# Kernel tuning notes

Measured on AMD Instinct MI355X. Metric: run time of the kernel, lower is better.

The kernel has to match this reference:

```python
import jax, jax.numpy as jnp
import numpy as np

SEQ_LEN = 96
D_MODEL = 512
BATCH = 512
FREQ = SEQ_LEN // 2 + 1  # 49
EPS = 1e-5


def setup_inputs() -> dict:
    key = jax.random.key(0)
    ks = jax.random.split(key, 9)
    s = 1.0 / np.sqrt(D_MODEL)
    return {
        "x": jax.random.normal(ks[0], (BATCH, SEQ_LEN, D_MODEL), jnp.float32),
        "freq_weights": jnp.ones((FREQ,), jnp.float32),
        "Wl": jax.random.normal(ks[1], (D_MODEL, D_MODEL), jnp.float32) * s,
        "bl": jax.random.normal(ks[2], (D_MODEL,), jnp.float32) * s,
        "Wh": jax.random.normal(ks[3], (D_MODEL, D_MODEL), jnp.float32) * s,
        "bh": jax.random.normal(ks[4], (D_MODEL,), jnp.float32) * s,
        "Wg": jax.random.normal(ks[5], (2 * D_MODEL, D_MODEL), jnp.float32) * s,
        "bg": jax.random.normal(ks[6], (D_MODEL,), jnp.float32) * s,
        "gamma": jnp.ones((D_MODEL,), jnp.float32),
        "beta": jnp.zeros((D_MODEL,), jnp.float32),
    }


def reference(x, freq_weights, Wl, bl, Wh, bh, Wg, bg, gamma, beta):
    # Batched rfft over seq axis for all channels at once: [B, F, D] complex
    xf = jnp.fft.rfft(x, axis=1)
    xw = xf * freq_weights[None, :, None]
    cutoff = FREQ // 3  # 16 (static)
    idx = jnp.arange(FREQ)[None, :, None]
    x_low_f = jnp.where(idx < cutoff, xw, 0)
    x_high_f = jnp.where(idx >= cutoff, xw, 0)
    x_low = jnp.fft.irfft(x_low_f, n=SEQ_LEN, axis=1)   # [B, S, D]
    x_high = jnp.fft.irfft(x_high_f, n=SEQ_LEN, axis=1)
    x_low = jnp.einsum("bsd,de->bse", x_low, Wl) + bl
    x_high = jnp.einsum("bsd,de->bse", x_high, Wh) + bh
    gate_in = jnp.concatenate([x_low, x_high], axis=-1)  # [B, S, 2D]
    gate = jax.nn.sigmoid(jnp.einsum("bsd,de->bse", gate_in, Wg) + bg)
    out = gate * x_low + (1.0 - gate) * x_high
    y = x + out  # dropout is identity in eval mode
    mu = jnp.mean(y, axis=-1, keepdims=True)
    var = jnp.var(y, axis=-1, keepdims=True)
    return (y - mu) / jnp.sqrt(var + EPS) * gamma + beta
```

## Files before the change

### kernel.cpp

```cpp
#include <hip/hip_runtime.h>

typedef unsigned short u16;
typedef unsigned int u32;

#define SEQ 96
#define DM 512
#define NBATCH 512
#define NFREQ 49
#define CUT 16
#define MROWS (NBATCH * SEQ)

typedef __attribute__((ext_vector_type(8))) short bf16x8;
typedef __attribute__((ext_vector_type(4))) float f32x4;

__device__ __forceinline__ u16 f2bf(float f) {
  u32 u = __float_as_uint(f);
  u32 r = (u + 0x7fffu + ((u >> 16) & 1u)) >> 16;
  return (u16)r;
}
__device__ __forceinline__ float bf2f(u16 u) {
  return __uint_as_float(((u32)u) << 16);
}

__device__ __forceinline__ void g2l16(const void* g, void* l) {
  __builtin_amdgcn_global_load_lds(
      (const __attribute__((address_space(1))) void*)g,
      (__attribute__((address_space(3))) void*)l, 16, 0, 0);
}

__global__ void build_filters_k(const float* __restrict__ w,
                                u16* __restrict__ FlB, u16* __restrict__ FhB) {
  int idx = blockIdx.x * 256 + threadIdx.x;
  if (idx >= SEQ * SEQ) return;
  int s = idx / SEQ, t = idx % SEQ;
  int d = s - t;
  const float scale = 1.0f / (float)SEQ;
  const float w0 = 6.283185307179586f / (float)SEQ;
  float cl = 0.f, ch = 0.f;
  for (int k = 0; k < NFREQ; k++) {
    int m = (k * d) % SEQ;
    if (m < 0) m += SEQ;
    float c = (k == 0 || k == SEQ / 2) ? 1.0f : 2.0f;
    float v = c * w[k] * cosf(w0 * (float)m) * scale;
    if (k < CUT) cl += v; else ch += v;
  }
  FlB[idx] = f2bf(cl);
  FhB[idx] = f2bf(ch);
}

__global__ void __launch_bounds__(256) transpose_w_k(
    const float* __restrict__ W, u16* __restrict__ Wt, int K, int N) {
  __shared__ float t[32][33];
  int k0 = blockIdx.x * 32, n0 = blockIdx.y * 32;
  int tx = threadIdx.x & 31, ty = threadIdx.x >> 5;
  #pragma unroll
  for (int r = 0; r < 32; r += 8)
    t[ty + r][tx] = W[(size_t)(k0 + ty + r) * N + n0 + tx];
  __syncthreads();
  #pragma unroll
  for (int r = 0; r < 32; r += 8)
    Wt[(size_t)(n0 + ty + r) * K + k0 + tx] = f2bf(t[tx][ty + r]);
}

__global__ void __launch_bounds__(256) filter_fused_k(
    const float* __restrict__ x, const u16* __restrict__ FlB,
    const u16* __restrict__ FhB, u16* __restrict__ xl, u16* __restrict__ xh) {
  __shared__ __align__(16) char ldsbuf[24576 + 12672];
  u16* Bs = (u16*)ldsbuf;
  float* xs = (float*)(ldsbuf + 24576);
  int tid = threadIdx.x;
  int lane = tid & 63, w = tid >> 6;
  int b = blockIdx.x, d0 = blockIdx.y * 128;

  const float* xb = x + (size_t)b * SEQ * DM + d0;
  u32* BsW = (u32*)Bs;
  #pragma unroll
  for (int q = 0; q < 4; q++) {
    #pragma unroll
    for (int v = 0; v < 3; v++) {
      int c = v * 256 + tid;
      int t = c >> 3, f = (c & 7) << 2;
      float4 fv = *(const float4*)(xb + (size_t)t * DM + q * 32 + f);
      xs[t * 33 + f + 0] = fv.x;
      xs[t * 33 + f + 1] = fv.y;
      xs[t * 33 + f + 2] = fv.z;
      xs[t * 33 + f + 3] = fv.w;
    }
    __syncthreads();
    #pragma unroll
    for (int v = 0; v < 6; v++) {
      int c = v * 256 + tid;
      int dl = c / 48, tw = c % 48;
      u32 lo = (u32)f2bf(xs[(2 * tw) * 33 + dl]);
      u32 hi = (u32)f2bf(xs[(2 * tw + 1) * 33 + dl]);
      BsW[(size_t)(q * 32 + dl) * 48 + tw] = lo | (hi << 16);
    }
    __syncthreads();
  }

  const int l15 = lane & 15, lq = lane >> 4;
  f32x4 acc[2][6][2] = {};
  #pragma unroll
  for (int ks = 0; ks < 3; ks++) {
    int kt = ks * 32;
    bf16x8 bfr[2];
    #pragma unroll
    for (int j = 0; j < 2; j++)
      bfr[j] = *(const bf16x8*)&Bs[(w * 32 + j * 16 + l15) * SEQ + kt + lq * 8];
    #pragma unroll
    for (int f = 0; f < 2; f++) {
      const u16* Fg = f ? FhB : FlB;
      #pragma unroll
      for (int i = 0; i < 6; i++) {
        bf16x8 afr = *(const bf16x8*)&Fg[(i * 16 + l15) * SEQ + kt + lq * 8];
        #pragma unroll
        for (int j = 0; j < 2; j++)
          acc[f][i][j] = __builtin_amdgcn_mfma_f32_16x16x32_bf16(afr, bfr[j], acc[f][i][j], 0, 0, 0);
      }
    }
  }
  __syncthreads();

  u16* T = (u16*)ldsbuf;
  u32* Tw = (u32*)ldsbuf;
  #pragma unroll
  for (int f = 0; f < 2; f++) {
    u16* dst = f ? xh : xl;
    #pragma unroll
    for (int i = 0; i < 6; i++)
      #pragma unroll
      for (int j = 0; j < 2; j++) {
        int d = w * 32 + j * 16 + l15;
        #pragma unroll
        for (int r = 0; r < 4; r++) {
          int s = i * 16 + lq * 4 + r;
          T[s * 130 + d] = f2bf(acc[f][i][j][r]);
        }
      }
    __syncthreads();
    u32* outw = (u32*)(dst + (size_t)b * SEQ * DM + d0);
    #pragma unroll
    for (int v = 0; v < 24; v++) {
      int c = v * 256 + tid;
      int s = c >> 6, dp = c & 63;
      outw[s * 256 + dp] = Tw[s * 65 + dp];
    }
    __syncthreads();
  }
}

__global__ void __launch_bounds__(256) gemm_proj_mfma_k(
    const u16* __restrict__ xl, const u16* __restrict__ xh,
    const u16* __restrict__ Wlt, const u16* __restrict__ Wht,
    const float* __restrict__ bl, const float* __restrict__ bh,
    u16* __restrict__ yl, u16* __restrict__ yh) {
  const u16* A = blockIdx.z ? xh : xl;
  const u16* Bt = blockIdx.z ? Wht : Wlt;
  const float* bias = blockIdx.z ? bh : bl;
  u16* C = blockIdx.z ? yh : yl;

  __shared__ __align__(16) u16 As[128 * 32];
  __shared__ __align__(16) u16 Bs[128 * 32];
  const int m0 = blockIdx.x * 128;
  const int n0 = blockIdx.y * 128;
  const int tid = threadIdx.x;
  const int lane = tid & 63;
  const int w = tid >> 6;
  const int wm = w & 1, wn = w >> 1;
  const int l15 = lane & 15;
  const int lq = lane >> 4;

  f32x4 acc[4][4] = {};

  for (int kt = 0; kt < 512; kt += 32) {
    #pragma unroll
    for (int r = 0; r < 2; r++) {
      int chunk = r * 256 + tid;
      int row = chunk >> 2;
      int ce = (chunk & 3) << 3;
      u32 lo = (u32)((r * 256 + w * 64) << 4);
      g2l16(A + (size_t)(m0 + row) * 512 + kt + ce, (char*)As + lo);
      g2l16(Bt + (size_t)(n0 + row) * 512 + kt + ce, (char*)Bs + lo);
    }
    __syncthreads();
    bf16x8 af[4], bf[4];
    #pragma unroll
    for (int i = 0; i < 4; i++)
      af[i] = *(const bf16x8*)&As[(wm * 64 + i * 16 + l15) * 32 + lq * 8];
    #pragma unroll
    for (int j = 0; j < 4; j++)
      bf[j] = *(const bf16x8*)&Bs[(wn * 64 + j * 16 + l15) * 32 + lq * 8];
    #pragma unroll
    for (int i = 0; i < 4; i++)
      #pragma unroll
      for (int j = 0; j < 4; j++)
        acc[i][j] = __builtin_amdgcn_mfma_f32_16x16x32_bf16(af[i], bf[j], acc[i][j], 0, 0, 0);
    __syncthreads();
  }

  #pragma unroll
  for (int j = 0; j < 4; j++) {
    int n = n0 + wn * 64 + j * 16 + l15;
    float bv = bias[n];
    #pragma unroll
    for (int i = 0; i < 4; i++) {
      int mrow = m0 + wm * 64 + i * 16 + lq * 4;
      #pragma unroll
      for (int r = 0; r < 4; r++)
        C[(size_t)(mrow + r) * 512 + n] = f2bf(acc[i][j][r] + bv);
    }
  }
}

__global__ void __launch_bounds__(256) gemm_gate_mfma_k(
    const u16* __restrict__ yl, const u16* __restrict__ yh,
    const u16* __restrict__ Wgt, const float* __restrict__ bg,
    u16* __restrict__ g) {
  __shared__ __align__(16) u16 As[128 * 32];
  __shared__ __align__(16) u16 Bs[128 * 32];
  const int m0 = blockIdx.x * 128;
  const int n0 = blockIdx.y * 128;
  const int tid = threadIdx.x;
  const int lane = tid & 63;
  const int w = tid >> 6;
  const int wm = w & 1, wn = w >> 1;
  const int l15 = lane & 15;
  const int lq = lane >> 4;

  f32x4 acc[4][4] = {};

  for (int kt = 0; kt < 1024; kt += 32) {
    const u16* Ak = (kt < 512) ? yl : yh;
    int ka = kt & 511;
    #pragma unroll
    for (int r = 0; r < 2; r++) {
      int chunk = r * 256 + tid;
      int row = chunk >> 2;
      int ce = (chunk & 3) << 3;
      u32 lo = (u32)((r * 256 + w * 64) << 4);
      g2l16(Ak + (size_t)(m0 + row) * 512 + ka + ce, (char*)As + lo);
      g2l16(Wgt + (size_t)(n0 + row) * 1024 + kt + ce, (char*)Bs + lo);
    }
    __syncthreads();
    bf16x8 af[4], bf[4];
    #pragma unroll
    for (int i = 0; i < 4; i++)
      af[i] = *(const bf16x8*)&As[(wm * 64 + i * 16 + l15) * 32 + lq * 8];
    #pragma unroll
    for (int j = 0; j < 4; j++)
      bf[j] = *(const bf16x8*)&Bs[(wn * 64 + j * 16 + l15) * 32 + lq * 8];
    #pragma unroll
    for (int i = 0; i < 4; i++)
      #pragma unroll
      for (int j = 0; j < 4; j++)
        acc[i][j] = __builtin_amdgcn_mfma_f32_16x16x32_bf16(af[i], bf[j], acc[i][j], 0, 0, 0);
    __syncthreads();
  }

  #pragma unroll
  for (int j = 0; j < 4; j++) {
    int n = n0 + wn * 64 + j * 16 + l15;
    float bv = bg[n];
    #pragma unroll
    for (int i = 0; i < 4; i++) {
      int mrow = m0 + wm * 64 + i * 16 + lq * 4;
      #pragma unroll
      for (int r = 0; r < 4; r++) {
        float z = acc[i][j][r] + bv;
        g[(size_t)(mrow + r) * 512 + n] = f2bf(1.0f / (1.0f + __expf(-z)));
      }
    }
  }
}

__global__ void __launch_bounds__(256) final_ln_k(
    const float* __restrict__ x, const u16* __restrict__ yl,
    const u16* __restrict__ yh, const u16* __restrict__ g,
    const float* __restrict__ gamma, const float* __restrict__ beta,
    float* __restrict__ out) {
  __shared__ float red[8];
  int r = blockIdx.x;
  size_t base = (size_t)r * 512;
  float vv[2];
  float sum = 0.f, sumsq = 0.f;
  #pragma unroll
  for (int j = 0; j < 2; j++) {
    int e = threadIdx.x + j * 256;
    float lv = bf2f(yl[base + e]);
    float hv = bf2f(yh[base + e]);
    float gv = bf2f(g[base + e]);
    float v = x[base + e] + gv * lv + (1.f - gv) * hv;
    vv[j] = v;
    sum += v;
    sumsq += v * v;
  }
  #pragma unroll
  for (int off = 32; off; off >>= 1) {
    sum += __shfl_down(sum, off);
    sumsq += __shfl_down(sumsq, off);
  }
  int wid = threadIdx.x >> 6;
  if ((threadIdx.x & 63) == 0) {
    red[wid] = sum;
    red[4 + wid] = sumsq;
  }
  __syncthreads();
  sum = red[0] + red[1] + red[2] + red[3];
  sumsq = red[4] + red[5] + red[6] + red[7];
  float mu = sum * (1.f / 512.f);
  float var = sumsq * (1.f / 512.f) - mu * mu;
  float inv = rsqrtf(var + 1e-5f);
  #pragma unroll
  for (int j = 0; j < 2; j++) {
    int e = threadIdx.x + j * 256;
    out[base + e] = (vv[j] - mu) * inv * gamma[e] + beta[e];
  }
}

extern "C" void kernel_launch(void* const* d_in, const int* in_sizes, int n_in,
                              void* d_out, int out_size, void* d_ws, size_t ws_size,
                              hipStream_t stream) {
  const float* x     = (const float*)d_in[0];
  const float* fw    = (const float*)d_in[1];
  const float* Wl    = (const float*)d_in[2];
  const float* bl    = (const float*)d_in[3];
  const float* Wh    = (const float*)d_in[4];
  const float* bh    = (const float*)d_in[5];
  const float* Wg    = (const float*)d_in[6];
  const float* bg    = (const float*)d_in[7];
  const float* gamma = (const float*)d_in[8];
  const float* beta  = (const float*)d_in[9];
  float* out = (float*)d_out;

  char* ws = (char*)d_ws;
  u16* FlB = (u16*)ws;
  u16* FhB = FlB + SEQ * SEQ;
  u16* Wlt = (u16*)(ws + 64 * 1024);
  u16* Wht = Wlt + 512 * 512;
  u16* Wgt = Wht + 512 * 512;
  size_t tsz = (size_t)MROWS * 512;
  u16* xl = (u16*)(ws + 4 * 1024 * 1024);
  u16* xh = xl + tsz;
  u16* yl = xh + tsz;
  u16* yh = yl + tsz;
  u16* gbuf = xl;

  build_filters_k<<<dim3(36), dim3(256), 0, stream>>>(fw, FlB, FhB);
  transpose_w_k<<<dim3(16, 16), dim3(256), 0, stream>>>(Wl, Wlt, 512, 512);
  transpose_w_k<<<dim3(16, 16), dim3(256), 0, stream>>>(Wh, Wht, 512, 512);
  transpose_w_k<<<dim3(32, 16), dim3(256), 0, stream>>>(Wg, Wgt, 1024, 512);
  filter_fused_k<<<dim3(NBATCH, DM / 128), dim3(256), 0, stream>>>(x, FlB, FhB, xl, xh);
  gemm_proj_mfma_k<<<dim3(MROWS / 128, 4, 2), dim3(256), 0, stream>>>(
      xl, xh, Wlt, Wht, bl, bh, yl, yh);
  gemm_gate_mfma_k<<<dim3(MROWS / 128, 4), dim3(256), 0, stream>>>(yl, yh, Wgt, bg, gbuf);
  final_ln_k<<<dim3(MROWS), dim3(256), 0, stream>>>(x, yl, yh, gbuf, gamma, beta, out);
}
```

Measured before the change: 454.5 us.

## Stage filters in LDS, store filter outputs directly, warp-per-row layernorm

The filter kernel now loads the low/high filter matrices into LDS via direct global-to-LDS loads instead of reading them from global per MFMA. It also drops the LDS transpose and writes bf16 results straight to global memory. The final layernorm kernel now handles one row per wave with vectorized 8-element loads and an xor-shuffle reduction, with no shared-memory barrier. The direct stores are narrower and less coalesced, and the async LDS loads rely on existing barriers for completion.

```diff
diff --git a/kernel.cpp b/kernel.cpp
--- a/kernel.cpp
+++ b/kernel.cpp
@@ -11,6 +11,7 @@
 #define MROWS (NBATCH * SEQ)
 
 typedef __attribute__((ext_vector_type(8))) short bf16x8;
+typedef __attribute__((ext_vector_type(8))) unsigned short u16x8;
 typedef __attribute__((ext_vector_type(4))) float f32x4;
 
 __device__ __forceinline__ u16 f2bf(float f) {
@@ -65,12 +66,19 @@
 __global__ void __launch_bounds__(256) filter_fused_k(
     const float* __restrict__ x, const u16* __restrict__ FlB,
     const u16* __restrict__ FhB, u16* __restrict__ xl, u16* __restrict__ xh) {
-  __shared__ __align__(16) char ldsbuf[24576 + 12672];
-  u16* Bs = (u16*)ldsbuf;
-  float* xs = (float*)(ldsbuf + 24576);
+  __shared__ __align__(16) u16 Bs[128 * SEQ];
+  __shared__ __align__(16) u16 As0[2 * SEQ * SEQ];
+  __shared__ float xs[SEQ * 33];
   int tid = threadIdx.x;
   int lane = tid & 63, w = tid >> 6;
   int b = blockIdx.x, d0 = blockIdx.y * 128;
+
+  #pragma unroll
+  for (int it = 0; it < 9; it++) {
+    int c = it * 256 + tid;
+    const u16* src = (c < 1152) ? (FlB + c * 8) : (FhB + (c - 1152) * 8);
+    g2l16(src, (char*)As0 + ((it * 256 + w * 64) << 4));
+  }
 
   const float* xb = x + (size_t)b * SEQ * DM + d0;
   u32* BsW = (u32*)Bs;
@@ -108,21 +116,15 @@
     for (int j = 0; j < 2; j++)
       bfr[j] = *(const bf16x8*)&Bs[(w * 32 + j * 16 + l15) * SEQ + kt + lq * 8];
     #pragma unroll
-    for (int f = 0; f < 2; f++) {
-      const u16* Fg = f ? FhB : FlB;
+    for (int f = 0; f < 2; f++)
       #pragma unroll
       for (int i = 0; i < 6; i++) {
-        bf16x8 afr = *(const bf16x8*)&Fg[(i * 16 + l15) * SEQ + kt + lq * 8];
+        bf16x8 afr = *(const bf16x8*)&As0[f * SEQ * SEQ + (i * 16 + l15) * SEQ + kt + lq * 8];
         #pragma unroll
         for (int j = 0; j < 2; j++)
           acc[f][i][j] = __builtin_amdgcn_mfma_f32_16x16x32_bf16(afr, bfr[j], acc[f][i][j], 0, 0, 0);
       }
-    }
-  }
-  __syncthreads();
-
-  u16* T = (u16*)ldsbuf;
-  u32* Tw = (u32*)ldsbuf;
+  }
   #pragma unroll
   for (int f = 0; f < 2; f++) {
     u16* dst = f ? xh : xl;
@@ -130,22 +132,13 @@
     for (int i = 0; i < 6; i++)
       #pragma unroll
       for (int j = 0; j < 2; j++) {
-        int d = w * 32 + j * 16 + l15;
+        int d = d0 + w * 32 + j * 16 + l15;
         #pragma unroll
         for (int r = 0; r < 4; r++) {
           int s = i * 16 + lq * 4 + r;
-          T[s * 130 + d] = f2bf(acc[f][i][j][r]);
+          dst[((size_t)b * SEQ + s) * DM + d] = f2bf(acc[f][i][j][r]);
         }
       }
-    __syncthreads();
-    u32* outw = (u32*)(dst + (size_t)b * SEQ * DM + d0);
-    #pragma unroll
-    for (int v = 0; v < 24; v++) {
-      int c = v * 256 + tid;
-      int s = c >> 6, dp = c & 63;
-      outw[s * 256 + dp] = Tw[s * 65 + dp];
-    }
-    __syncthreads();
   }
 }
 
@@ -278,43 +271,53 @@
     const u16* __restrict__ yh, const u16* __restrict__ g,
     const float* __restrict__ gamma, const float* __restrict__ beta,
     float* __restrict__ out) {
-  __shared__ float red[8];
-  int r = blockIdx.x;
-  size_t base = (size_t)r * 512;
-  float vv[2];
+  const int wave = threadIdx.x >> 6;
+  const int lane = threadIdx.x & 63;
+  const size_t row = (size_t)blockIdx.x * 4 + wave;
+  const size_t base = row * 512 + lane * 8;
+  const int e = lane * 8;
+
+  float4 xv0 = *(const float4*)(x + base);
+  float4 xv1 = *(const float4*)(x + base + 4);
+  u16x8 lv = *(const u16x8*)(yl + base);
+  u16x8 hv = *(const u16x8*)(yh + base);
+  u16x8 gv = *(const u16x8*)(g + base);
+
+  float v[8];
+  const float xs[8] = {xv0.x, xv0.y, xv0.z, xv0.w, xv1.x, xv1.y, xv1.z, xv1.w};
   float sum = 0.f, sumsq = 0.f;
   #pragma unroll
-  for (int j = 0; j < 2; j++) {
-    int e = threadIdx.x + j * 256;
-    float lv = bf2f(yl[base + e]);
-    float hv = bf2f(yh[base + e]);
-    float gv = bf2f(g[base + e]);
-    float v = x[base + e] + gv * lv + (1.f - gv) * hv;
-    vv[j] = v;
-    sum += v;
-    sumsq += v * v;
+  for (int k = 0; k < 8; k++) {
+    float gl = bf2f(gv[k]);
+    float vv = xs[k] + gl * bf2f(lv[k]) + (1.f - gl) * bf2f(hv[k]);
+    v[k] = vv;
+    sum += vv;
+    sumsq += vv * vv;
   }
   #pragma unroll
   for (int off = 32; off; off >>= 1) {
-    sum += __shfl_down(sum, off);
-    sumsq += __shfl_down(sumsq, off);
-  }
-  int wid = threadIdx.x >> 6;
-  if ((threadIdx.x & 63) == 0) {
-    red[wid] = sum;
-    red[4 + wid] = sumsq;
-  }
-  __syncthreads();
-  sum = red[0] + red[1] + red[2] + red[3];
-  sumsq = red[4] + red[5] + red[6] + red[7];
-  float mu = sum * (1.f / 512.f);
-  float var = sumsq * (1.f / 512.f) - mu * mu;
-  float inv = rsqrtf(var + 1e-5f);
-  #pragma unroll
-  for (int j = 0; j < 2; j++) {
-    int e = threadIdx.x + j * 256;
-    out[base + e] = (vv[j] - mu) * inv * gamma[e] + beta[e];
-  }
+    sum += __shfl_xor(sum, off);
+    sumsq += __shfl_xor(sumsq, off);
+  }
+  const float mu = sum * (1.f / 512.f);
+  const float var = sumsq * (1.f / 512.f) - mu * mu;
+  const float inv = rsqrtf(var + 1e-5f);
+
+  float4 gm0 = *(const float4*)(gamma + e);
+  float4 gm1 = *(const float4*)(gamma + e + 4);
+  float4 bt0 = *(const float4*)(beta + e);
+  float4 bt1 = *(const float4*)(beta + e + 4);
+  float4 o0, o1;
+  o0.x = (v[0] - mu) * inv * gm0.x + bt0.x;
+  o0.y = (v[1] - mu) * inv * gm0.y + bt0.y;
+  o0.z = (v[2] - mu) * inv * gm0.z + bt0.z;
+  o0.w = (v[3] - mu) * inv * gm0.w + bt0.w;
+  o1.x = (v[4] - mu) * inv * gm1.x + bt1.x;
+  o1.y = (v[5] - mu) * inv * gm1.y + bt1.y;
+  o1.z = (v[6] - mu) * inv * gm1.z + bt1.z;
+  o1.w = (v[7] - mu) * inv * gm1.w + bt1.w;
+  *(float4*)(out + base) = o0;
+  *(float4*)(out + base + 4) = o1;
 }
 
 extern "C" void kernel_launch(void* const* d_in, const int* in_sizes, int n_in,
@@ -353,5 +356,5 @@
   gemm_proj_mfma_k<<<dim3(MROWS / 128, 4, 2), dim3(256), 0, stream>>>(
       xl, xh, Wlt, Wht, bl, bh, yl, yh);
   gemm_gate_mfma_k<<<dim3(MROWS / 128, 4), dim3(256), 0, stream>>>(yl, yh, Wgt, bg, gbuf);
-  final_ln_k<<<dim3(MROWS), dim3(256), 0, stream>>>(x, yl, yh, gbuf, gamma, beta, out);
-}
+  final_ln_k<<<dim3(MROWS / 4), dim3(256), 0, stream>>>(x, yl, yh, gbuf, gamma, beta, out);
+}
```

Result: faster. 441.5 us (-2.9%).
